# Kernel tuning notes

Measured on AMD Instinct MI355X. Metric: run time of the kernel, lower is better.

Reference implementation:

```python
import jax, jax.numpy as jnp
from jax import lax
import numpy as np

D = 128          # condition_dim
NUM_STEPS = 1000
FFN = 2048       # torch TransformerEncoderLayer default dim_feedforward


def _conv(x, w, b):
    # 3x3 conv, stride 1, padding 1 (SAME), NCHW / OIHW layout as in torch
    y = lax.conv_general_dilated(x, w, (1, 1), 'SAME',
                                 dimension_numbers=('NCHW', 'OIHW', 'NCHW'))
    return y + b[None, :, None, None]


def _ln(x, g, b):
    m = jnp.mean(x, -1, keepdims=True)
    v = jnp.mean((x - m) ** 2, -1, keepdims=True)
    return (x - m) / jnp.sqrt(v + 1e-5) * g + b


def setup_inputs() -> dict:
    key = jax.random.key(0)
    ks = iter(jax.random.split(key, 40))
    B, C, H, W = 64, 3, 128, 128
    flat = C * H * W
    def rn(shape, scale=0.02):
        return jax.random.normal(next(ks), shape, jnp.float32) * scale
    return dict(
        cond_img=jax.random.normal(next(ks), (B, C, H, W), jnp.float32),
        tgt_img=jax.random.normal(next(ks), (B, C, H, W), jnp.float32),
        noise=jax.random.normal(next(ks), (B, C, H, W), jnp.float32),
        t=jax.random.randint(next(ks), (B,), 0, NUM_STEPS),
        # condition encoder params
        enc_lin_w=rn((D, flat)), enc_lin_b=jnp.zeros((D,), jnp.float32),
        in_w=rn((2, 3 * D, D)), in_b=jnp.zeros((2, 3 * D), jnp.float32),
        out_w=rn((2, D, D)), out_b=jnp.zeros((2, D), jnp.float32),
        ff1_w=rn((2, FFN, D)), ff1_b=jnp.zeros((2, FFN), jnp.float32),
        ff2_w=rn((2, D, FFN)), ff2_b=jnp.zeros((2, D), jnp.float32),
        ln1_g=jnp.ones((2, D), jnp.float32), ln1_b=jnp.zeros((2, D), jnp.float32),
        ln2_g=jnp.ones((2, D), jnp.float32), ln2_b=jnp.zeros((2, D), jnp.float32),
        # SimpleUNet params
        d1_w=rn((32, C, 3, 3)), d1_b=jnp.zeros((32,), jnp.float32),
        d2_w=rn((64, 32, 3, 3)), d2_b=jnp.zeros((64,), jnp.float32),
        mid_w=rn((64, D)), mid_b=jnp.zeros((64,), jnp.float32),
        u1_w=rn((32, 64, 3, 3)), u1_b=jnp.zeros((32,), jnp.float32),
        u2_w=rn((C, 32, 3, 3)), u2_b=jnp.zeros((C,), jnp.float32),
    )


def _forward(cond_img, tgt_img, noise, t,
             enc_lin_w, enc_lin_b, in_w, in_b, out_w, out_b,
             ff1_w, ff1_b, ff2_w, ff2_b, ln1_g, ln1_b, ln2_g, ln2_b,
             d1_w, d1_b, d2_w, d2_b, mid_w, mid_b, u1_w, u1_b, u2_w, u2_b):
    B = cond_img.shape[0]
    # ---- TransformerConditionEncoder (seq_len == 1, eval mode) ----
    x = cond_img.reshape(B, -1) @ enc_lin_w.T + enc_lin_b  # [B, D]
    for i in range(2):
        # self-attention over a length-1 sequence: softmax over one key == 1,
        # so attn(x) == out_proj(v_proj(x)) exactly.
        v = x @ in_w[i][2 * D:3 * D].T + in_b[i][2 * D:3 * D]
        a = v @ out_w[i].T + out_b[i]
        x = _ln(x + a, ln1_g[i], ln1_b[i])
        f = jnp.maximum(x @ ff1_w[i].T + ff1_b[i], 0.0) @ ff2_w[i].T + ff2_b[i]
        x = _ln(x + f, ln2_g[i], ln2_b[i])
    c = x  # [B, D]
    # ---- LinearScheduler.q_sample ----
    betas = jnp.linspace(1e-4, 0.02, NUM_STEPS)
    alpha_bars = jnp.cumprod(1.0 - betas)
    ab = alpha_bars[t][:, None, None, None]
    z_t = jnp.sqrt(ab) * tgt_img + jnp.sqrt(1.0 - ab) * noise
    # ---- SimpleUNet ----
    h = jax.nn.relu(_conv(z_t, d1_w, d1_b))
    h = jax.nn.relu(_conv(h, d2_w, d2_b))
    h = h + (c @ mid_w.T + mid_b)[:, :, None, None]
    h = jax.nn.relu(_conv(h, u1_w, u1_b))
    eps_pred = _conv(h, u2_w, u2_b)
    # ---- MSE loss ----
    return jnp.mean((eps_pred - noise) ** 2)


def reference(cond_img, tgt_img, noise, t,
              enc_lin_w, enc_lin_b, in_w, in_b, out_w, out_b,
              ff1_w, ff1_b, ff2_w, ff2_b, ln1_g, ln1_b, ln2_g, ln2_b,
              d1_w, d1_b, d2_w, d2_b, mid_w, mid_b, u1_w, u1_b, u2_w, u2_b):
    return _forward(cond_img, tgt_img, noise, t,
                    enc_lin_w, enc_lin_b, in_w, in_b, out_w, out_b,
                    ff1_w, ff1_b, ff2_w, ff2_b, ln1_g, ln1_b, ln2_g, ln2_b,
                    d1_w, d1_b, d2_w, d2_b, mid_w, mid_b, u1_w, u1_b, u2_w, u2_b)
```

## Files before the change

kernel.cpp:

```cpp
#include <hip/hip_runtime.h>
#include <math.h>

#define ENC_K 49152
#define KSEG 64
#define KLEN (ENC_K / KSEG)

typedef __attribute__((ext_vector_type(8))) short bf16x8;
typedef __attribute__((ext_vector_type(4))) float f32x4;

__device__ inline unsigned short f2bf(float f) {
    unsigned int u = __builtin_bit_cast(unsigned int, f);
    unsigned int r = u + 0x7fffu + ((u >> 16) & 1u);
    return (unsigned short)(r >> 16);
}
__device__ inline float bf2f(unsigned short h) {
    return __builtin_bit_cast(float, ((unsigned int)h) << 16);
}
__device__ inline float dot4(const float4 a, const float4 b) {
    return a.x * b.x + a.y * b.y + a.z * b.z + a.w * b.w;
}

__global__ void k_alpha(const int* __restrict__ t, float* __restrict__ sab, float* __restrict__ snab) {
    int b = threadIdx.x;
    if (b < 64) {
        int tb = t[b];
        const float step = (0.02f - 1e-4f) / 999.0f;
        float ab = 1.0f;
        for (int i = 0; i <= tb; ++i) {
            float beta = 1e-4f + step * (float)i;
            ab *= (1.0f - beta);
        }
        sab[b] = sqrtf(ab);
        snab[b] = sqrtf(1.0f - ab);
    }
}

__global__ void k_prep_cw(const float* __restrict__ w, unsigned short* __restrict__ out, int CO, int CI) {
    int idx = blockIdx.x * 256 + threadIdx.x;
    int total = CO * CI * 9;
    if (idx < total) {
        int tap = idx / (CO * CI);
        int rem = idx % (CO * CI);
        int co = rem / CI, ci = rem % CI;
        out[idx] = f2bf(w[((size_t)co * CI + ci) * 9 + tap]);
    }
}

__global__ void k_prep_u2(const float* __restrict__ w, unsigned short* __restrict__ out) {
    int idx = blockIdx.x * 256 + threadIdx.x;
    if (idx < 9 * 16 * 32) {
        int tap = idx / 512;
        int rem = idx % 512;
        int co = rem / 32, ci = rem % 32;
        out[idx] = (co < 3) ? f2bf(w[((size_t)co * 32 + ci) * 9 + tap]) : (unsigned short)0;
    }
}

__global__ void k_prep_bf(const float* __restrict__ in, unsigned short* __restrict__ out, int n) {
    int i = blockIdx.x * 256 + threadIdx.x;
    if (i < n) out[i] = f2bf(in[i]);
}

__global__ void k_enc_gemm(const float* __restrict__ cond, const float* __restrict__ w,
                           float* __restrict__ partial) {
    __shared__ float As[32][68];
    __shared__ float Ws[32][68];
    int tid = threadIdx.x;
    int j = tid & 15, i = tid >> 4;
    int d0 = blockIdx.x * 32, b0 = blockIdx.y * 32;
    int k0 = blockIdx.z * KLEN;
    float a00 = 0.f, a01 = 0.f, a10 = 0.f, a11 = 0.f;
    for (int kk = 0; kk < KLEN; kk += 64) {
        for (int idx = tid; idx < 512; idx += 256) {
            int r = idx >> 4, c = (idx & 15) << 2;
            *(float4*)&As[r][c] = *(const float4*)&cond[(size_t)(b0 + r) * ENC_K + k0 + kk + c];
            *(float4*)&Ws[r][c] = *(const float4*)&w[(size_t)(d0 + r) * ENC_K + k0 + kk + c];
        }
        __syncthreads();
        const float4* aA = (const float4*)&As[i][0];
        const float4* aB = (const float4*)&As[i + 16][0];
        const float4* wA = (const float4*)&Ws[j][0];
        const float4* wB = (const float4*)&Ws[j + 16][0];
#pragma unroll
        for (int k = 0; k < 16; ++k) {
            float4 av0 = aA[k], av1 = aB[k], wv0 = wA[k], wv1 = wB[k];
            a00 += dot4(av0, wv0); a01 += dot4(av0, wv1);
            a10 += dot4(av1, wv0); a11 += dot4(av1, wv1);
        }
        __syncthreads();
    }
    size_t base = (size_t)blockIdx.z * 64;
    partial[(base + b0 + i) * 128 + d0 + j] = a00;
    partial[(base + b0 + i) * 128 + d0 + j + 16] = a01;
    partial[(base + b0 + i + 16) * 128 + d0 + j] = a10;
    partial[(base + b0 + i + 16) * 128 + d0 + j + 16] = a11;
}

__global__ void k_enc_reduce(const float* __restrict__ partial, const float* __restrict__ bias,
                             float* __restrict__ x0) {
    int idx = blockIdx.x * 256 + threadIdx.x;
    float s = bias[idx & 127];
    for (int ks = 0; ks < KSEG; ++ks) s += partial[(size_t)ks * 8192 + idx];
    x0[idx] = s;
}

__device__ float sum128(float v, int tid, float* red) {
    if (tid < 128) red[tid] = v;
    __syncthreads();
    if (tid < 64) red[tid] += red[tid + 64]; __syncthreads();
    if (tid < 32) red[tid] += red[tid + 32]; __syncthreads();
    if (tid < 16) red[tid] += red[tid + 16]; __syncthreads();
    if (tid < 8)  red[tid] += red[tid + 8];  __syncthreads();
    if (tid < 4)  red[tid] += red[tid + 4];  __syncthreads();
    if (tid < 2)  red[tid] += red[tid + 2];  __syncthreads();
    if (tid < 1)  red[tid] += red[tid + 1];  __syncthreads();
    float s = red[0];
    __syncthreads();
    return s;
}

__global__ __launch_bounds__(512) void k_tf_attn(
    const float* __restrict__ xs, float* __restrict__ yo,
    const float* __restrict__ in_w, const float* __restrict__ in_b,
    const float* __restrict__ out_w, const float* __restrict__ out_b,
    const float* __restrict__ ln1_g, const float* __restrict__ ln1_b, int L) {
    __shared__ float xr[128], vr[128], tp[4][128], red[128];
    int b = blockIdx.x, tid = threadIdx.x;
    if (tid < 128) xr[tid] = xs[b * 128 + tid];
    __syncthreads();
    int d = tid & 127, s = tid >> 7;
    {
        const float4* w = (const float4*)(in_w + ((size_t)L * 384 + 256 + d) * 128) + s * 8;
        const float4* x4 = (const float4*)xr + s * 8;
        float p = 0.f;
#pragma unroll
        for (int k = 0; k < 8; ++k) p += dot4(x4[k], w[k]);
        tp[s][d] = p;
    }
    __syncthreads();
    if (tid < 128) vr[tid] = in_b[L * 384 + 256 + tid] + tp[0][tid] + tp[1][tid] + tp[2][tid] + tp[3][tid];
    __syncthreads();
    {
        const float4* w = (const float4*)(out_w + ((size_t)L * 128 + d) * 128) + s * 8;
        const float4* v4 = (const float4*)vr + s * 8;
        float p = 0.f;
#pragma unroll
        for (int k = 0; k < 8; ++k) p += dot4(v4[k], w[k]);
        tp[s][d] = p;
    }
    __syncthreads();
    float y = 0.f;
    if (tid < 128) y = xr[tid] + out_b[L * 128 + tid] + tp[0][tid] + tp[1][tid] + tp[2][tid] + tp[3][tid];
    float m1 = sum128(y, tid, red) * (1.f / 128.f);
    float c1 = y - m1;
    float v1 = sum128(c1 * c1, tid, red) * (1.f / 128.f);
    if (tid < 128)
        yo[b * 128 + tid] = c1 * rsqrtf(v1 + 1e-5f) * ln1_g[L * 128 + tid] + ln1_b[L * 128 + tid];
}

__global__ __launch_bounds__(256, 2) void k_ff1m(
    const float* __restrict__ yo, const unsigned short* __restrict__ w1b,
    const float* __restrict__ ff1_b, unsigned short* __restrict__ f1, int L) {
    __shared__ __align__(16) unsigned short xs[64 * 136];
    int tid = threadIdx.x;
    int lane = tid & 63, wv = tid >> 6, l15 = lane & 15, ch = lane >> 4;
    int n0 = blockIdx.x * 64 + wv * 16;
    for (int e = tid; e < 8192; e += 256)
        xs[(e >> 7) * 136 + (e & 127)] = f2bf(yo[e]);
    __syncthreads();
    f32x4 acc[4];
    f32x4 zf = {0.f, 0.f, 0.f, 0.f};
#pragma unroll
    for (int rg = 0; rg < 4; ++rg) acc[rg] = zf;
    const unsigned short* wrow = w1b + ((size_t)L * 2048 + n0 + l15) * 128 + ch * 8;
#pragma unroll
    for (int ks = 0; ks < 4; ++ks) {
        bf16x8 af = *(const bf16x8*)(wrow + ks * 32);
#pragma unroll
        for (int rg = 0; rg < 4; ++rg) {
            bf16x8 bv = *(const bf16x8*)(xs + (rg * 16 + l15) * 136 + ks * 32 + ch * 8);
            acc[rg] = __builtin_amdgcn_mfma_f32_16x16x32_bf16(af, bv, acc[rg], 0, 0, 0);
        }
    }
#pragma unroll
    for (int rg = 0; rg < 4; ++rg) {
        ushort4 o;
#pragma unroll
        for (int r = 0; r < 4; ++r)
            ((unsigned short*)&o)[r] =
                f2bf(fmaxf(acc[rg][r] + ff1_b[L * 2048 + n0 + ch * 4 + r], 0.f));
        *(ushort4*)(f1 + (size_t)(rg * 16 + l15) * 2056 + n0 + ch * 4) = o;
    }
}

__global__ __launch_bounds__(256, 2) void k_ff2m(
    const unsigned short* __restrict__ f1, const unsigned short* __restrict__ w2b,
    float* __restrict__ part, int L) {
    int tid = threadIdx.x;
    int lane = tid & 63, wv = tid >> 6, l15 = lane & 15, ch = lane >> 4;
    int ks = blockIdx.x;
    int dw = blockIdx.y * 64 + wv * 16;
    f32x4 acc[4];
    f32x4 zf = {0.f, 0.f, 0.f, 0.f};
#pragma unroll
    for (int rg = 0; rg < 4; ++rg) acc[rg] = zf;
    const unsigned short* wrow = w2b + ((size_t)L * 128 + dw + l15) * 2048 + ks * 512 + ch * 8;
    const unsigned short* frow = f1 + ks * 512 + ch * 8;
#pragma unroll
    for (int kst = 0; kst < 16; ++kst) {
        bf16x8 af = *(const bf16x8*)(wrow + kst * 32);
#pragma unroll
        for (int rg = 0; rg < 4; ++rg) {
            bf16x8 bv = *(const bf16x8*)(frow + (size_t)(rg * 16 + l15) * 2056 + kst * 32);
            acc[rg] = __builtin_amdgcn_mfma_f32_16x16x32_bf16(af, bv, acc[rg], 0, 0, 0);
        }
    }
#pragma unroll
    for (int rg = 0; rg < 4; ++rg)
        *(float4*)&part[((size_t)ks * 64 + rg * 16 + l15) * 128 + dw + ch * 4] = *(float4*)&acc[rg];
}

__global__ __launch_bounds__(128) void k_tf_red(
    const float* __restrict__ part, const float* __restrict__ yo,
    float* __restrict__ xs, const float* __restrict__ ff2_b,
    const float* __restrict__ ln2_g, const float* __restrict__ ln2_b, int L) {
    __shared__ float red[128];
    int b = blockIdx.x, tid = threadIdx.x;
    float y2 = yo[b * 128 + tid] + ff2_b[L * 128 + tid];
#pragma unroll
    for (int ks = 0; ks < 4; ++ks) y2 += part[((size_t)ks * 64 + b) * 128 + tid];
    float m2 = sum128(y2, tid, red) * (1.f / 128.f);
    float c2 = y2 - m2;
    float v2 = sum128(c2 * c2, tid, red) * (1.f / 128.f);
    xs[b * 128 + tid] = c2 * rsqrtf(v2 + 1e-5f) * ln2_g[L * 128 + tid] + ln2_b[L * 128 + tid];
}

__global__ void k_mid(const float* __restrict__ xe, const float* __restrict__ mid_w,
                      const float* __restrict__ mid_b, float* __restrict__ mid) {
    int b = blockIdx.x, c = threadIdx.x;
    float s = mid_b[c];
    const float* xr = xe + b * 128;
    const float* wr = mid_w + c * 128;
    for (int k = 0; k < 128; ++k) s += xr[k] * wr[k];
    mid[b * 64 + c] = s;
}

__global__ __launch_bounds__(256, 4) void k_conv1(
    const float* __restrict__ tgt, const float* __restrict__ noise,
    const float* __restrict__ sab, const float* __restrict__ snab,
    const float* __restrict__ wgt, const float* __restrict__ bias,
    unsigned short* __restrict__ h1, int b0) {
    __shared__ float it[3][34][35];
    __shared__ float wt[8][3][9];
    int tid = threadIdx.x;
    int tx = tid & 7, ty = tid >> 3;
    int bx = blockIdx.x, by = blockIdx.y;
    int bl = blockIdx.z >> 2, g = blockIdx.z & 3;
    int bg = b0 + bl, co0 = g * 8;
    float za = sab[bg], zb = snab[bg];
    for (int idx = tid; idx < 3 * 34 * 34; idx += 256) {
        int c = idx / 1156, rem = idx % 1156;
        int yy = rem / 34, xx = rem % 34;
        int gy = by * 32 + yy - 1, gx = bx * 32 + xx - 1;
        float v = 0.f;
        if (gy >= 0 && gy < 128 && gx >= 0 && gx < 128) {
            size_t off = (((size_t)bg * 3 + c) * 128 + gy) * 128 + gx;
            v = za * tgt[off] + zb * noise[off];
        }
        it[c][yy][xx] = v;
    }
    for (int idx = tid; idx < 8 * 27; idx += 256) {
        int co = idx / 27, rem = idx % 27;
        wt[co][rem / 9][rem % 9] = wgt[(size_t)(co0 + co) * 27 + rem];
    }
    __syncthreads();
    float acc[8][4];
#pragma unroll
    for (int co = 0; co < 8; ++co)
#pragma unroll
        for (int p = 0; p < 4; ++p) acc[co][p] = 0.f;
#pragma unroll
    for (int c = 0; c < 3; ++c)
#pragma unroll
        for (int ky = 0; ky < 3; ++ky) {
            float win[6];
#pragma unroll
            for (int i = 0; i < 6; ++i) win[i] = it[c][ty + ky][tx * 4 + i];
#pragma unroll
            for (int kx = 0; kx < 3; ++kx)
#pragma unroll
                for (int co = 0; co < 8; ++co) {
                    float w = wt[co][c][ky * 3 + kx];
#pragma unroll
                    for (int p = 0; p < 4; ++p) acc[co][p] += win[kx + p] * w;
                }
        }
    int gy = by * 32 + ty, gx0 = bx * 32 + tx * 4;
#pragma unroll
    for (int p = 0; p < 4; ++p) {
        ushort4 oa, ob;
#pragma unroll
        for (int co = 0; co < 4; ++co)
            ((unsigned short*)&oa)[co] = f2bf(fmaxf(acc[co][p] + bias[co0 + co], 0.f));
#pragma unroll
        for (int co = 0; co < 4; ++co)
            ((unsigned short*)&ob)[co] = f2bf(fmaxf(acc[co + 4][p] + bias[co0 + co + 4], 0.f));
        size_t o = (((size_t)bl * 128 + gy) * 128 + gx0 + p) * 32 + co0;
        *(ushort4*)(h1 + o) = oa;
        *(ushort4*)(h1 + o + 4) = ob;
    }
}

template <int CIN, int COB, int COUT, int MOUT>
__global__ __launch_bounds__(256, 2) void k_convMg(
    const unsigned short* __restrict__ in, const unsigned short* __restrict__ wb,
    const float* __restrict__ bias, const float* __restrict__ mid,
    unsigned short* __restrict__ out, int b0) {
    const int GROUPS = COUT / (16 * COB);
    __shared__ __align__(16) unsigned short in_t[10 * 34 * 40];
    __shared__ __align__(16) unsigned short w_t[9 * COB * 16 * 40];
    int tid = threadIdx.x;
    int bx = blockIdx.x, by = blockIdx.y;
    int bl = blockIdx.z / GROUPS, g = blockIdx.z % GROUPS;
    int bg = b0 + bl;
    int co0 = g * COB * 16;
    int lane = tid & 63, wv = tid >> 6;
    int l15 = lane & 15, ch = lane >> 4;

    f32x4 acc[2][2][COB];
    f32x4 zf = {0.f, 0.f, 0.f, 0.f};
#pragma unroll
    for (int a = 0; a < 2; ++a)
#pragma unroll
        for (int bq = 0; bq < 2; ++bq)
#pragma unroll
            for (int c = 0; c < COB; ++c) acc[a][bq][c] = zf;

    for (int cs = 0; cs < CIN / 32; ++cs) {
        if (cs) __syncthreads();
        for (int c = tid; c < 10 * 34 * 4; c += 256) {
            int cc = c & 3, pix = c >> 2;
            int xx = pix % 34, yy = pix / 34;
            int gy = by * 8 + yy - 1, gx = bx * 32 + xx - 1;
            bf16x8 v = {0, 0, 0, 0, 0, 0, 0, 0};
            if (gy >= 0 && gy < 128 && gx >= 0 && gx < 128)
                v = *(const bf16x8*)(in + (((size_t)bl * 128 + gy) * 128 + gx) * CIN + cs * 32 + cc * 8);
            *(bf16x8*)(in_t + pix * 40 + cc * 8) = v;
        }
        for (int c = tid; c < 9 * COB * 16 * 4; c += 256) {
            int cc = c & 3, row = c >> 2;
            int tap = row / (COB * 16), co = row % (COB * 16);
            bf16x8 v = *(const bf16x8*)(wb + ((size_t)(tap * COUT + co0 + co)) * CIN + cs * 32 + cc * 8);
            *(bf16x8*)(w_t + row * 40 + cc * 8) = v;
        }
        __syncthreads();
#pragma unroll
        for (int ky = 0; ky < 3; ++ky)
#pragma unroll
            for (int kx = 0; kx < 3; ++kx) {
                int tap = ky * 3 + kx;
                bf16x8 af[COB];
#pragma unroll
                for (int cb = 0; cb < COB; ++cb)
                    af[cb] = *(const bf16x8*)(w_t + (tap * COB * 16 + cb * 16 + l15) * 40 + ch * 8);
#pragma unroll
                for (int yl = 0; yl < 2; ++yl) {
                    int yloc = 2 * wv + yl + ky;
#pragma unroll
                    for (int xt = 0; xt < 2; ++xt) {
                        int xloc = xt * 16 + l15 + kx;
                        bf16x8 bfv = *(const bf16x8*)(in_t + (yloc * 34 + xloc) * 40 + ch * 8);
#pragma unroll
                        for (int cb = 0; cb < COB; ++cb)
                            acc[yl][xt][cb] = __builtin_amdgcn_mfma_f32_16x16x32_bf16(
                                af[cb], bfv, acc[yl][xt][cb], 0, 0, 0);
                    }
                }
            }
    }
#pragma unroll
    for (int yl = 0; yl < 2; ++yl) {
        int gy = by * 8 + 2 * wv + yl;
#pragma unroll
        for (int xt = 0; xt < 2; ++xt) {
            int gx = bx * 32 + xt * 16 + l15;
            size_t pixo = (((size_t)bl * 128 + gy) * 128 + gx) * COUT;
#pragma unroll
            for (int cb = 0; cb < COB; ++cb) {
                int co = co0 + cb * 16 + ch * 4;
                ushort4 o;
#pragma unroll
                for (int r = 0; r < 4; ++r) {
                    float v = acc[yl][xt][cb][r] + bias[co + r];
                    v = fmaxf(v, 0.f);
                    if (MOUT == 2) v += mid[bg * 64 + co + r];
                    ((unsigned short*)&o)[r] = f2bf(v);
                }
                *(ushort4*)(out + pixo + co) = o;
            }
        }
    }
}

__global__ __launch_bounds__(256, 3) void k_u2m(
    const unsigned short* __restrict__ h3, const unsigned short* __restrict__ wbu2,
    const float* __restrict__ u2_b, const float* __restrict__ noise,
    float* __restrict__ partial, int b0) {
    __shared__ __align__(16) unsigned short in_t[340 * 40];
    __shared__ __align__(16) unsigned short w_t[9 * 16 * 40];
    __shared__ float rs[256];
    int tid = threadIdx.x;
    int bx = blockIdx.x, by = blockIdx.y, bl = blockIdx.z;
    int bg = b0 + bl;
    int lane = tid & 63, wv = tid >> 6, l15 = lane & 15, ch = lane >> 4;

    for (int c = tid; c < 340 * 4; c += 256) {
        int cc = c & 3, pix = c >> 2;
        int xx = pix % 34, yy = pix / 34;
        int gy = by * 8 + yy - 1, gx = bx * 32 + xx - 1;
        bf16x8 v = {0, 0, 0, 0, 0, 0, 0, 0};
        if (gy >= 0 && gy < 128 && gx >= 0 && gx < 128)
            v = *(const bf16x8*)(h3 + (((size_t)bl * 128 + gy) * 128 + gx) * 32 + cc * 8);
        *(bf16x8*)(in_t + pix * 40 + cc * 8) = v;
    }
    for (int c = tid; c < 9 * 16 * 4; c += 256) {
        int cc = c & 3, row = c >> 2;
        bf16x8 v = *(const bf16x8*)(wbu2 + (size_t)row * 32 + cc * 8);
        *(bf16x8*)(w_t + row * 40 + cc * 8) = v;
    }
    __syncthreads();

    f32x4 acc[2][2];
    f32x4 zf = {0.f, 0.f, 0.f, 0.f};
    acc[0][0] = zf; acc[0][1] = zf; acc[1][0] = zf; acc[1][1] = zf;
#pragma unroll
    for (int ky = 0; ky < 3; ++ky)
#pragma unroll
        for (int kx = 0; kx < 3; ++kx) {
            int tap = ky * 3 + kx;
            bf16x8 af = *(const bf16x8*)(w_t + (tap * 16 + l15) * 40 + ch * 8);
#pragma unroll
            for (int yl = 0; yl < 2; ++yl) {
                int yloc = 2 * wv + yl + ky;
#pragma unroll
                for (int xt = 0; xt < 2; ++xt) {
                    int xloc = xt * 16 + l15 + kx;
                    bf16x8 bfv = *(const bf16x8*)(in_t + (yloc * 34 + xloc) * 40 + ch * 8);
                    acc[yl][xt] = __builtin_amdgcn_mfma_f32_16x16x32_bf16(af, bfv, acc[yl][xt], 0, 0, 0);
                }
            }
        }
    float ss = 0.f;
    if (ch == 0) {
#pragma unroll
        for (int yl = 0; yl < 2; ++yl) {
            int gy = by * 8 + 2 * wv + yl;
#pragma unroll
            for (int xt = 0; xt < 2; ++xt) {
                int gx = bx * 32 + xt * 16 + l15;
#pragma unroll
                for (int r = 0; r < 3; ++r) {
                    float v = acc[yl][xt][r] + u2_b[r];
                    float d = v - noise[(((size_t)bg * 3 + r) * 128 + gy) * 128 + gx];
                    ss += d * d;
                }
            }
        }
    }
    rs[tid] = ss;
    __syncthreads();
    for (int s = 128; s > 0; s >>= 1) {
        if (tid < s) rs[tid] += rs[tid + s];
        __syncthreads();
    }
    if (tid == 0) partial[bg * 64 + by * 4 + bx] = rs[0];
}

__global__ void k_final(const float* __restrict__ partial, float* __restrict__ out) {
    __shared__ float rs[256];
    int tid = threadIdx.x;
    float s = 0.f;
    for (int i = tid; i < 4096; i += 256) s += partial[i];
    rs[tid] = s;
    __syncthreads();
    for (int st = 128; st > 0; st >>= 1) {
        if (tid < st) rs[tid] += rs[tid + st];
        __syncthreads();
    }
    if (tid == 0) out[0] = rs[0] / 3145728.0f;
}

extern "C" void kernel_launch(void* const* d_in, const int* in_sizes, int n_in,
                              void* d_out, int out_size, void* d_ws, size_t ws_size,
                              hipStream_t stream) {
    const float* cond   = (const float*)d_in[0];
    const float* tgt    = (const float*)d_in[1];
    const float* noise  = (const float*)d_in[2];
    const int*   t      = (const int*)d_in[3];
    const float* enc_w  = (const float*)d_in[4];
    const float* enc_b  = (const float*)d_in[5];
    const float* in_w   = (const float*)d_in[6];
    const float* in_b   = (const float*)d_in[7];
    const float* out_w  = (const float*)d_in[8];
    const float* out_b  = (const float*)d_in[9];
    const float* ff1_w  = (const float*)d_in[10];
    const float* ff1_b  = (const float*)d_in[11];
    const float* ff2_w  = (const float*)d_in[12];
    const float* ff2_b  = (const float*)d_in[13];
    const float* ln1_g  = (const float*)d_in[14];
    const float* ln1_b  = (const float*)d_in[15];
    const float* ln2_g  = (const float*)d_in[16];
    const float* ln2_b  = (const float*)d_in[17];
    const float* d1_w   = (const float*)d_in[18];
    const float* d1_b   = (const float*)d_in[19];
    const float* d2_w   = (const float*)d_in[20];
    const float* d2_b   = (const float*)d_in[21];
    const float* mid_w  = (const float*)d_in[22];
    const float* mid_b  = (const float*)d_in[23];
    const float* u1_w   = (const float*)d_in[24];
    const float* u1_b   = (const float*)d_in[25];
    const float* u2_w   = (const float*)d_in[26];
    const float* u2_b   = (const float*)d_in[27];

    float* ws = (float*)d_ws;
    float* sab     = ws;
    float* snab    = ws + 64;
    float* x0      = ws + 128;
    float* mid     = ws + 16512;
    float* msepart = ws + 86144;
    unsigned short* wb2  = (unsigned short*)(ws + 90240);
    unsigned short* wbu1 = (unsigned short*)(ws + 99456);
    unsigned short* wbu2 = (unsigned short*)(ws + 108672);

    const size_t SMALL = 131072;
    const size_t ENCP = (size_t)KSEG * 8192;
    float* encpart = ws + SMALL;
    float* tfy     = encpart + ENCP;
    unsigned short* tff1 = (unsigned short*)(tfy + 8192);
    float* tfpart  = tfy + 8192 + 65792;
    unsigned short* wbf1 = (unsigned short*)(tfpart + 32768);
    unsigned short* wbf2 = (unsigned short*)(tfpart + 32768 + 262144);

    size_t fixed = SMALL + ENCP + 8192 + 65792 + 32768 + 262144 + 262144;
    size_t avail = (ws_size / 4 > fixed) ? (ws_size / 4 - fixed) : 0;
    int NB = 1;
    const int cands[7] = {64, 32, 16, 8, 4, 2, 1};
    for (int ci = 0; ci < 7; ++ci) {
        if ((size_t)cands[ci] * 1048576ull <= avail) { NB = cands[ci]; break; }
    }
    unsigned short* hb1 = (unsigned short*)(ws + fixed);
    unsigned short* hb2 = (unsigned short*)(ws + fixed + (size_t)NB * 262144ull);
    unsigned short* hb3 = (unsigned short*)(ws + fixed + (size_t)NB * 786432ull);

    k_alpha<<<1, 64, 0, stream>>>(t, sab, snab);
    k_prep_cw<<<72, 256, 0, stream>>>(d2_w, wb2, 64, 32);
    k_prep_cw<<<72, 256, 0, stream>>>(u1_w, wbu1, 32, 64);
    k_prep_u2<<<18, 256, 0, stream>>>(u2_w, wbu2);
    k_prep_bf<<<2048, 256, 0, stream>>>(ff1_w, wbf1, 524288);
    k_prep_bf<<<2048, 256, 0, stream>>>(ff2_w, wbf2, 524288);
    k_enc_gemm<<<dim3(4, 2, KSEG), 256, 0, stream>>>(cond, enc_w, encpart);
    k_enc_reduce<<<32, 256, 0, stream>>>(encpart, enc_b, x0);
    for (int L = 0; L < 2; ++L) {
        k_tf_attn<<<64, 512, 0, stream>>>(x0, tfy, in_w, in_b, out_w, out_b, ln1_g, ln1_b, L);
        k_ff1m<<<32, 256, 0, stream>>>(tfy, wbf1, ff1_b, tff1, L);
        k_ff2m<<<dim3(4, 2), 256, 0, stream>>>(tff1, wbf2, tfpart, L);
        k_tf_red<<<64, 128, 0, stream>>>(tfpart, tfy, x0, ff2_b, ln2_g, ln2_b, L);
    }
    k_mid<<<64, 64, 0, stream>>>(x0, mid_w, mid_b, mid);

    for (int cb = 0; cb < 64; cb += NB) {
        k_conv1<<<dim3(4, 4, NB * 4), 256, 0, stream>>>(
            tgt, noise, sab, snab, d1_w, d1_b, hb1, cb);
        k_convMg<32, 4, 64, 2><<<dim3(4, 16, NB), 256, 0, stream>>>(
            hb1, wb2, d2_b, mid, hb2, cb);
        k_convMg<64, 2, 32, 1><<<dim3(4, 16, NB), 256, 0, stream>>>(
            hb2, wbu1, u1_b, nullptr, hb3, cb);
        k_u2m<<<dim3(4, 16, NB), 256, 0, stream>>>(
            hb3, wbu2, u2_b, noise, msepart, cb);
    }

    k_final<<<1, 256, 0, stream>>>(msepart, (float*)d_out);
}
```

Measured before the change: 399.2 us.

## Load conv weights directly into registers and split output channels across blocks

```diff
diff --git a/kernel.cpp b/kernel.cpp
--- a/kernel.cpp
+++ b/kernel.cpp
@@ -311,30 +311,29 @@
     }
 }
 
-template <int CIN, int COB, int COUT, int MOUT>
-__global__ __launch_bounds__(256, 2) void k_convMg(
+template <int CIN, int COUT, int MOUT>
+__global__ __launch_bounds__(256, 4) void k_convR(
     const unsigned short* __restrict__ in, const unsigned short* __restrict__ wb,
     const float* __restrict__ bias, const float* __restrict__ mid,
     unsigned short* __restrict__ out, int b0) {
-    const int GROUPS = COUT / (16 * COB);
+    const int GROUPS = COUT / 32;
     __shared__ __align__(16) unsigned short in_t[10 * 34 * 40];
-    __shared__ __align__(16) unsigned short w_t[9 * COB * 16 * 40];
     int tid = threadIdx.x;
     int bx = blockIdx.x, by = blockIdx.y;
     int bl = blockIdx.z / GROUPS, g = blockIdx.z % GROUPS;
     int bg = b0 + bl;
-    int co0 = g * COB * 16;
+    int co0 = g * 32;
     int lane = tid & 63, wv = tid >> 6;
     int l15 = lane & 15, ch = lane >> 4;
 
-    f32x4 acc[2][2][COB];
+    f32x4 acc[2][2][2];
     f32x4 zf = {0.f, 0.f, 0.f, 0.f};
 #pragma unroll
     for (int a = 0; a < 2; ++a)
 #pragma unroll
         for (int bq = 0; bq < 2; ++bq)
 #pragma unroll
-            for (int c = 0; c < COB; ++c) acc[a][bq][c] = zf;
+            for (int c = 0; c < 2; ++c) acc[a][bq][c] = zf;
 
     for (int cs = 0; cs < CIN / 32; ++cs) {
         if (cs) __syncthreads();
@@ -347,22 +346,18 @@
                 v = *(const bf16x8*)(in + (((size_t)bl * 128 + gy) * 128 + gx) * CIN + cs * 32 + cc * 8);
             *(bf16x8*)(in_t + pix * 40 + cc * 8) = v;
         }
-        for (int c = tid; c < 9 * COB * 16 * 4; c += 256) {
-            int cc = c & 3, row = c >> 2;
-            int tap = row / (COB * 16), co = row % (COB * 16);
-            bf16x8 v = *(const bf16x8*)(wb + ((size_t)(tap * COUT + co0 + co)) * CIN + cs * 32 + cc * 8);
-            *(bf16x8*)(w_t + row * 40 + cc * 8) = v;
-        }
         __syncthreads();
 #pragma unroll
-        for (int ky = 0; ky < 3; ++ky)
+        for (int ky = 0; ky < 3; ++ky) {
+            bf16x8 wreg[3][2];
+#pragma unroll
+            for (int kx = 0; kx < 3; ++kx)
+#pragma unroll
+                for (int cb = 0; cb < 2; ++cb)
+                    wreg[kx][cb] = *(const bf16x8*)(
+                        wb + ((size_t)((ky * 3 + kx) * COUT + co0 + cb * 16 + l15)) * CIN + cs * 32 + ch * 8);
 #pragma unroll
             for (int kx = 0; kx < 3; ++kx) {
-                int tap = ky * 3 + kx;
-                bf16x8 af[COB];
-#pragma unroll
-                for (int cb = 0; cb < COB; ++cb)
-                    af[cb] = *(const bf16x8*)(w_t + (tap * COB * 16 + cb * 16 + l15) * 40 + ch * 8);
 #pragma unroll
                 for (int yl = 0; yl < 2; ++yl) {
                     int yloc = 2 * wv + yl + ky;
@@ -371,12 +366,13 @@
                         int xloc = xt * 16 + l15 + kx;
                         bf16x8 bfv = *(const bf16x8*)(in_t + (yloc * 34 + xloc) * 40 + ch * 8);
 #pragma unroll
-                        for (int cb = 0; cb < COB; ++cb)
+                        for (int cb = 0; cb < 2; ++cb)
                             acc[yl][xt][cb] = __builtin_amdgcn_mfma_f32_16x16x32_bf16(
-                                af[cb], bfv, acc[yl][xt][cb], 0, 0, 0);
+                                wreg[kx][cb], bfv, acc[yl][xt][cb], 0, 0, 0);
                     }
                 }
             }
+        }
     }
 #pragma unroll
     for (int yl = 0; yl < 2; ++yl) {
@@ -386,7 +382,7 @@
             int gx = bx * 32 + xt * 16 + l15;
             size_t pixo = (((size_t)bl * 128 + gy) * 128 + gx) * COUT;
 #pragma unroll
-            for (int cb = 0; cb < COB; ++cb) {
+            for (int cb = 0; cb < 2; ++cb) {
                 int co = co0 + cb * 16 + ch * 4;
                 ushort4 o;
 #pragma unroll
@@ -571,9 +567,9 @@
     for (int cb = 0; cb < 64; cb += NB) {
         k_conv1<<<dim3(4, 4, NB * 4), 256, 0, stream>>>(
             tgt, noise, sab, snab, d1_w, d1_b, hb1, cb);
-        k_convMg<32, 4, 64, 2><<<dim3(4, 16, NB), 256, 0, stream>>>(
+        k_convR<32, 64, 2><<<dim3(4, 16, NB * 2), 256, 0, stream>>>(
             hb1, wb2, d2_b, mid, hb2, cb);
-        k_convMg<64, 2, 32, 1><<<dim3(4, 16, NB), 256, 0, stream>>>(
+        k_convR<64, 32, 1><<<dim3(4, 16, NB), 256, 0, stream>>>(
             hb2, wbu1, u1_b, nullptr, hb3, cb);
         k_u2m<<<dim3(4, 16, NB), 256, 0, stream>>>(
             hb3, wbu2, u2_b, noise, msepart, cb);
```

Measured after the change: 448.4 us. 1.12x slower.

## Retile conv1 to 16 output channels and remap blocks for XCD locality

Applied to the files above, without the earlier changes.

```diff
diff --git a/kernel.cpp b/kernel.cpp
--- a/kernel.cpp
+++ b/kernel.cpp
@@ -18,6 +18,11 @@
 }
 __device__ inline float dot4(const float4 a, const float4 b) {
     return a.x * b.x + a.y * b.y + a.z * b.z + a.w * b.w;
+}
+
+__device__ inline int xcd_work(int total) {
+    int orig = blockIdx.x + gridDim.x * (blockIdx.y + gridDim.y * blockIdx.z);
+    return (orig & 7) * (total >> 3) + (orig >> 3);
 }
 
 __global__ void k_alpha(const int* __restrict__ t, float* __restrict__ sab, float* __restrict__ snab) {
@@ -250,18 +255,21 @@
     const float* __restrict__ sab, const float* __restrict__ snab,
     const float* __restrict__ wgt, const float* __restrict__ bias,
     unsigned short* __restrict__ h1, int b0) {
-    __shared__ float it[3][34][35];
-    __shared__ float wt[8][3][9];
-    int tid = threadIdx.x;
-    int tx = tid & 7, ty = tid >> 3;
-    int bx = blockIdx.x, by = blockIdx.y;
-    int bl = blockIdx.z >> 2, g = blockIdx.z & 3;
-    int bg = b0 + bl, co0 = g * 8;
+    __shared__ float it[3][18][35];
+    __shared__ float wt[16][3][9];
+    int tid = threadIdx.x;
+    int tx = tid & 15, ty = tid >> 4;
+    int total = gridDim.x * gridDim.y * gridDim.z;
+    int w = xcd_work(total);
+    int bx = w % gridDim.x; int t2 = w / gridDim.x;
+    int by = t2 % gridDim.y; int bz = t2 / gridDim.y;
+    int bl = bz >> 1, g = bz & 1;
+    int bg = b0 + bl, co0 = g * 16;
     float za = sab[bg], zb = snab[bg];
-    for (int idx = tid; idx < 3 * 34 * 34; idx += 256) {
-        int c = idx / 1156, rem = idx % 1156;
+    for (int idx = tid; idx < 3 * 18 * 34; idx += 256) {
+        int c = idx / (18 * 34), rem = idx % (18 * 34);
         int yy = rem / 34, xx = rem % 34;
-        int gy = by * 32 + yy - 1, gx = bx * 32 + xx - 1;
+        int gy = by * 16 + yy - 1, gx = bx * 32 + xx - 1;
         float v = 0.f;
         if (gy >= 0 && gy < 128 && gx >= 0 && gx < 128) {
             size_t off = (((size_t)bg * 3 + c) * 128 + gy) * 128 + gx;
@@ -269,45 +277,40 @@
         }
         it[c][yy][xx] = v;
     }
-    for (int idx = tid; idx < 8 * 27; idx += 256) {
+    for (int idx = tid; idx < 16 * 27; idx += 256) {
         int co = idx / 27, rem = idx % 27;
         wt[co][rem / 9][rem % 9] = wgt[(size_t)(co0 + co) * 27 + rem];
     }
     __syncthreads();
-    float acc[8][4];
-#pragma unroll
-    for (int co = 0; co < 8; ++co)
-#pragma unroll
-        for (int p = 0; p < 4; ++p) acc[co][p] = 0.f;
+    float acc[16][2];
+#pragma unroll
+    for (int co = 0; co < 16; ++co) { acc[co][0] = 0.f; acc[co][1] = 0.f; }
 #pragma unroll
     for (int c = 0; c < 3; ++c)
 #pragma unroll
         for (int ky = 0; ky < 3; ++ky) {
-            float win[6];
-#pragma unroll
-            for (int i = 0; i < 6; ++i) win[i] = it[c][ty + ky][tx * 4 + i];
+            float win[4];
+#pragma unroll
+            for (int i = 0; i < 4; ++i) win[i] = it[c][ty + ky][tx * 2 + i];
 #pragma unroll
             for (int kx = 0; kx < 3; ++kx)
 #pragma unroll
-                for (int co = 0; co < 8; ++co) {
-                    float w = wt[co][c][ky * 3 + kx];
-#pragma unroll
-                    for (int p = 0; p < 4; ++p) acc[co][p] += win[kx + p] * w;
+                for (int co = 0; co < 16; ++co) {
+                    float ww = wt[co][c][ky * 3 + kx];
+                    acc[co][0] += win[kx] * ww;
+                    acc[co][1] += win[kx + 1] * ww;
                 }
         }
-    int gy = by * 32 + ty, gx0 = bx * 32 + tx * 4;
-#pragma unroll
-    for (int p = 0; p < 4; ++p) {
-        ushort4 oa, ob;
-#pragma unroll
-        for (int co = 0; co < 4; ++co)
-            ((unsigned short*)&oa)[co] = f2bf(fmaxf(acc[co][p] + bias[co0 + co], 0.f));
-#pragma unroll
-        for (int co = 0; co < 4; ++co)
-            ((unsigned short*)&ob)[co] = f2bf(fmaxf(acc[co + 4][p] + bias[co0 + co + 4], 0.f));
+    int gy = by * 16 + ty, gx0 = bx * 32 + tx * 2;
+#pragma unroll
+    for (int p = 0; p < 2; ++p) {
+        __attribute__((aligned(16))) unsigned short ov[16];
+#pragma unroll
+        for (int co = 0; co < 16; ++co)
+            ov[co] = f2bf(fmaxf(acc[co][p] + bias[co0 + co], 0.f));
         size_t o = (((size_t)bl * 128 + gy) * 128 + gx0 + p) * 32 + co0;
-        *(ushort4*)(h1 + o) = oa;
-        *(ushort4*)(h1 + o + 4) = ob;
+        *(float4*)(h1 + o) = *(float4*)&ov[0];
+        *(float4*)(h1 + o + 8) = *(float4*)&ov[8];
     }
 }
 
@@ -320,8 +323,11 @@
     __shared__ __align__(16) unsigned short in_t[10 * 34 * 40];
     __shared__ __align__(16) unsigned short w_t[9 * COB * 16 * 40];
     int tid = threadIdx.x;
-    int bx = blockIdx.x, by = blockIdx.y;
-    int bl = blockIdx.z / GROUPS, g = blockIdx.z % GROUPS;
+    int total = gridDim.x * gridDim.y * gridDim.z;
+    int wk = xcd_work(total);
+    int bx = wk % gridDim.x; int t2 = wk / gridDim.x;
+    int by = t2 % gridDim.y; int bz = t2 / gridDim.y;
+    int bl = bz / GROUPS, g = bz % GROUPS;
     int bg = b0 + bl;
     int co0 = g * COB * 16;
     int lane = tid & 63, wv = tid >> 6;
@@ -410,7 +416,10 @@
     __shared__ __align__(16) unsigned short w_t[9 * 16 * 40];
     __shared__ float rs[256];
     int tid = threadIdx.x;
-    int bx = blockIdx.x, by = blockIdx.y, bl = blockIdx.z;
+    int total = gridDim.x * gridDim.y * gridDim.z;
+    int wk = xcd_work(total);
+    int bx = wk % gridDim.x; int t2 = wk / gridDim.x;
+    int by = t2 % gridDim.y; int bl = t2 / gridDim.y;
     int bg = b0 + bl;
     int lane = tid & 63, wv = tid >> 6, l15 = lane & 15, ch = lane >> 4;
 
@@ -569,7 +578,7 @@
     k_mid<<<64, 64, 0, stream>>>(x0, mid_w, mid_b, mid);
 
     for (int cb = 0; cb < 64; cb += NB) {
-        k_conv1<<<dim3(4, 4, NB * 4), 256, 0, stream>>>(
+        k_conv1<<<dim3(4, 8, NB * 2), 256, 0, stream>>>(
             tgt, noise, sab, snab, d1_w, d1_b, hb1, cb);
         k_convMg<32, 4, 64, 2><<<dim3(4, 16, NB), 256, 0, stream>>>(
             hb1, wb2, d2_b, mid, hb2, cb);
```

New measurement: 388.1 us. -2.8%, faster.
